# Optimization experiments

Hardware: AMD Instinct MI355X
Metric: run time of the kernel (lower is better)

Reference implementation:

```python
import jax, jax.numpy as jnp
import numpy as np

B = 65536        # batch
L = 1024         # input_size
K = 16           # filter_size
NUM_CLASSES = 4


def setup_inputs() -> dict:
    key = jax.random.key(0)
    k1, k2, k3, k4 = jax.random.split(key, 4)
    x = jax.random.normal(k1, (B, 1, L), dtype=jnp.float32)
    w = jax.random.normal(k2, (1, 1, K), dtype=jnp.float32) * 0.1
    b = jax.random.normal(k3, (1,), dtype=jnp.float32) * 0.1
    # per-class (lo, hi) intervals, lo <= hi, non-negative so sqrt fallback is real
    ranges = jnp.sort(jax.random.uniform(k4, (NUM_CLASSES, 2), dtype=jnp.float32) * 2.0, axis=1)
    return {"x": x, "w": w, "b": b, "ranges": ranges}


def reference(x, w, b, ranges):
    # Conv1d(1->1, K) + bias, ReLU, MaxPool1d over the full valid length -> [B,1,1]
    y = jax.lax.conv_general_dilated(
        x, w, window_strides=(1,), padding='VALID',
        dimension_numbers=('NCH', 'OIH', 'NCH'))
    y = jnp.maximum(y + b[None, :, None], 0.0)
    v = jnp.max(y, axis=-1, keepdims=True)            # [B,1,1]

    # vectorized replacement of Tensor.apply_(from_ranges_to_output)
    lo = ranges[:, 0]                                  # [4]
    hi = ranges[:, 1]                                  # [4]
    vv = v[..., None]                                  # [B,1,1,1]
    matches = (vv >= lo) & (vv <= hi)                  # [B,1,1,4]
    in_any = jnp.any(matches, axis=-1)                 # [B,1,1]
    first_match = jnp.argmax(matches, axis=-1)         # first i with v in [lo_i,hi_i]

    # fallback: distances (v^2 + bound)^0.5 over interleaved [lo0,hi0,lo1,hi1,...]
    flat_bounds = ranges.reshape(-1)                   # [8]
    dists = jnp.sqrt(vv * vv + flat_bounds)            # [B,1,1,8]
    fallback_label = jnp.argmin(dists, axis=-1) // 2   # [B,1,1]

    out = jnp.where(in_any, first_match, fallback_label).astype(jnp.uint8)
    return out
```

## Files before the change

### kernel.cpp

```cpp
#include <hip/hip_runtime.h>
#include <math.h>

#define BROWS 65536
#define LLEN  1024
#define KW    16
#define NPOS  (LLEN - KW + 1)
#define RPB   4
#define NBLOCKS 2048
#define ROWS_PER_WAVE (BROWS / (NBLOCKS * RPB))

typedef float f4 __attribute__((ext_vector_type(4)));

__device__ __forceinline__ void load_row(const float* __restrict__ xr,
                                         int fbase, float* __restrict__ buf) {
#pragma unroll
    for (int j = 0; j < 8; ++j) {
        int off = fbase + 4 * j;
        off = (off > LLEN - 4) ? (LLEN - 4) : off;
        *(f4*)(&buf[4 * j]) = *(const f4*)(xr + off);
    }
}

__device__ __forceinline__ float conv_max(const float* __restrict__ xv,
                                          const float* __restrict__ wv,
                                          int own) {
    float vmax = -INFINITY;
#pragma unroll
    for (int pp = 0; pp < KW; ++pp) {
        float acc = 0.0f;
#pragma unroll
        for (int k = 0; k < KW; ++k) acc = fmaf(xv[pp + k], wv[k], acc);
        if (own + pp < NPOS) vmax = fmaxf(vmax, acc);
    }
    return vmax;
}

__device__ __forceinline__ void finish_row(float vmax, int lane, float bv,
                                           const float* __restrict__ lo,
                                           const float* __restrict__ hi,
                                           int fb, int* __restrict__ out,
                                           int row) {
#pragma unroll
    for (int off = 32; off > 0; off >>= 1)
        vmax = fmaxf(vmax, __shfl_xor(vmax, off, 64));
    if (lane == 0) {
        const float v = fmaxf(vmax + bv, 0.0f);
        int label = fb;
#pragma unroll
        for (int j = 3; j >= 0; --j)
            label = (v >= lo[j] && v <= hi[j]) ? j : label;
        out[row] = label;
    }
}

__global__ __launch_bounds__(256) void conv_pool_classify(
    const float* __restrict__ x,
    const float* __restrict__ w,
    const float* __restrict__ bias,
    const float* __restrict__ ranges,
    int* __restrict__ out)
{
    const int lane  = threadIdx.x & 63;
    const int wid   = threadIdx.x >> 6;
    const int wave  = blockIdx.x * RPB + wid;
    const int row0  = wave * ROWS_PER_WAVE;
    const int fbase = 16 * lane;

    float wv[KW];
#pragma unroll
    for (int k = 0; k < KW; ++k) wv[k] = w[k];
    const float bv = bias[0];

    float rr[8];
#pragma unroll
    for (int j = 0; j < 8; ++j) rr[j] = ranges[j];
    int fb = 0; float bm = rr[0];
#pragma unroll
    for (int j = 1; j < 8; ++j) { if (rr[j] < bm) { bm = rr[j]; fb = j; } }
    fb >>= 1;
    const float lo[4] = {rr[0], rr[2], rr[4], rr[6]};
    const float hi[4] = {rr[1], rr[3], rr[5], rr[7]};

    float bufA[32], bufB[32];
    load_row(x + (size_t)row0 * LLEN, fbase, bufA);

#pragma unroll 1
    for (int it = 0; it < ROWS_PER_WAVE; it += 2) {
        load_row(x + (size_t)(row0 + it + 1) * LLEN, fbase, bufB);
        const float m0 = conv_max(bufA, wv, fbase);
        finish_row(m0, lane, bv, lo, hi, fb, out, row0 + it);

        if (it + 2 < ROWS_PER_WAVE)
            load_row(x + (size_t)(row0 + it + 2) * LLEN, fbase, bufA);
        const float m1 = conv_max(bufB, wv, fbase);
        finish_row(m1, lane, bv, lo, hi, fb, out, row0 + it + 1);
    }
}

extern "C" void kernel_launch(void* const* d_in, const int* in_sizes, int n_in,
                              void* d_out, int out_size, void* d_ws, size_t ws_size,
                              hipStream_t stream) {
    const float* x      = (const float*)d_in[0];
    const float* w      = (const float*)d_in[1];
    const float* bias   = (const float*)d_in[2];
    const float* ranges = (const float*)d_in[3];
    int* out = (int*)d_out;

    dim3 grid(NBLOCKS);
    dim3 block(256);
    conv_pool_classify<<<grid, block, 0, stream>>>(x, w, bias, ranges, out);
}
```

Measured before the change: 361.0 us.

## Stage rows through swizzled LDS with coalesced nontemporal loads and batched label stores

Each wave now loads a row with fully coalesced nontemporal float4 loads (64 lanes over contiguous 1 KB segments) instead of overlapping per-lane 128-byte windows. The data is written to a swizzled shared-memory tile, and each lane reads back its 32-float window for the 16-tap convolution. Labels are collected in one register per lane and written with a single store per wave. This is meant to cut redundant global traffic and improve coalescing, at the cost of LDS round trips and barrier-free reuse that relies on wave-local ordering.

```diff
diff --git a/kernel.cpp b/kernel.cpp
--- a/kernel.cpp
+++ b/kernel.cpp
@@ -9,49 +9,9 @@
 #define NBLOCKS 2048
 #define ROWS_PER_WAVE (BROWS / (NBLOCKS * RPB))
 
-typedef float f4 __attribute__((ext_vector_type(4)));
+typedef float nt_float4 __attribute__((ext_vector_type(4)));
 
-__device__ __forceinline__ void load_row(const float* __restrict__ xr,
-                                         int fbase, float* __restrict__ buf) {
-#pragma unroll
-    for (int j = 0; j < 8; ++j) {
-        int off = fbase + 4 * j;
-        off = (off > LLEN - 4) ? (LLEN - 4) : off;
-        *(f4*)(&buf[4 * j]) = *(const f4*)(xr + off);
-    }
-}
-
-__device__ __forceinline__ float conv_max(const float* __restrict__ xv,
-                                          const float* __restrict__ wv,
-                                          int own) {
-    float vmax = -INFINITY;
-#pragma unroll
-    for (int pp = 0; pp < KW; ++pp) {
-        float acc = 0.0f;
-#pragma unroll
-        for (int k = 0; k < KW; ++k) acc = fmaf(xv[pp + k], wv[k], acc);
-        if (own + pp < NPOS) vmax = fmaxf(vmax, acc);
-    }
-    return vmax;
-}
-
-__device__ __forceinline__ void finish_row(float vmax, int lane, float bv,
-                                           const float* __restrict__ lo,
-                                           const float* __restrict__ hi,
-                                           int fb, int* __restrict__ out,
-                                           int row) {
-#pragma unroll
-    for (int off = 32; off > 0; off >>= 1)
-        vmax = fmaxf(vmax, __shfl_xor(vmax, off, 64));
-    if (lane == 0) {
-        const float v = fmaxf(vmax + bv, 0.0f);
-        int label = fb;
-#pragma unroll
-        for (int j = 3; j >= 0; --j)
-            label = (v >= lo[j] && v <= hi[j]) ? j : label;
-        out[row] = label;
-    }
-}
+__device__ __forceinline__ int swz(int g) { return g ^ ((g >> 3) & 7); }
 
 __global__ __launch_bounds__(256) void conv_pool_classify(
     const float* __restrict__ x,
@@ -60,11 +20,12 @@
     const float* __restrict__ ranges,
     int* __restrict__ out)
 {
-    const int lane  = threadIdx.x & 63;
-    const int wid   = threadIdx.x >> 6;
-    const int wave  = blockIdx.x * RPB + wid;
-    const int row0  = wave * ROWS_PER_WAVE;
-    const int fbase = 16 * lane;
+    __shared__ nt_float4 lds[RPB][LLEN / 4];
+
+    const int lane = threadIdx.x & 63;
+    const int wid  = threadIdx.x >> 6;
+    const int wave = blockIdx.x * RPB + wid;
+    const int row0 = wave * ROWS_PER_WAVE;
 
     float wv[KW];
 #pragma unroll
@@ -81,20 +42,59 @@
     const float lo[4] = {rr[0], rr[2], rr[4], rr[6]};
     const float hi[4] = {rr[1], rr[3], rr[5], rr[7]};
 
-    float bufA[32], bufB[32];
-    load_row(x + (size_t)row0 * LLEN, fbase, bufA);
+    nt_float4 p[4];
+    {
+        const float* __restrict__ xr = x + (size_t)row0 * LLEN;
+#pragma unroll
+        for (int s = 0; s < 4; ++s)
+            p[s] = __builtin_nontemporal_load((const nt_float4*)(xr + 256 * s + 4 * lane));
+    }
 
-#pragma unroll 1
-    for (int it = 0; it < ROWS_PER_WAVE; it += 2) {
-        load_row(x + (size_t)(row0 + it + 1) * LLEN, fbase, bufB);
-        const float m0 = conv_max(bufA, wv, fbase);
-        finish_row(m0, lane, bv, lo, hi, fb, out, row0 + it);
+    int mylbl = 0;
 
-        if (it + 2 < ROWS_PER_WAVE)
-            load_row(x + (size_t)(row0 + it + 2) * LLEN, fbase, bufA);
-        const float m1 = conv_max(bufB, wv, fbase);
-        finish_row(m1, lane, bv, lo, hi, fb, out, row0 + it + 1);
+    for (int it = 0; it < ROWS_PER_WAVE; ++it) {
+#pragma unroll
+        for (int s = 0; s < 4; ++s)
+            lds[wid][swz(64 * s + lane)] = p[s];
+
+        if (it + 1 < ROWS_PER_WAVE) {
+            const float* __restrict__ xr = x + (size_t)(row0 + it + 1) * LLEN;
+#pragma unroll
+            for (int s = 0; s < 4; ++s)
+                p[s] = __builtin_nontemporal_load((const nt_float4*)(xr + 256 * s + 4 * lane));
+        }
+
+        float xv[32];
+#pragma unroll
+        for (int j = 0; j < 8; ++j) {
+            int g = 4 * lane + j;
+            if (g > 255) g = 255;
+            *(nt_float4*)(&xv[4 * j]) = lds[wid][swz(g)];
+        }
+
+        const int own = 16 * lane;
+        float vmax = -INFINITY;
+#pragma unroll
+        for (int pp = 0; pp < KW; ++pp) {
+            float acc = 0.0f;
+#pragma unroll
+            for (int k = 0; k < KW; ++k) acc = fmaf(xv[pp + k], wv[k], acc);
+            vmax = ((own + pp) < NPOS) ? fmaxf(vmax, acc) : vmax;
+        }
+
+#pragma unroll
+        for (int off = 32; off > 0; off >>= 1)
+            vmax = fmaxf(vmax, __shfl_xor(vmax, off, 64));
+
+        const float v = fmaxf(vmax + bv, 0.0f);
+        int label = fb;
+#pragma unroll
+        for (int j = 3; j >= 0; --j)
+            label = (v >= lo[j] && v <= hi[j]) ? j : label;
+        if (lane == it) mylbl = label;
     }
+
+    if (lane < ROWS_PER_WAVE) out[row0 + lane] = mylbl;
 }
 
 extern "C" void kernel_launch(void* const* d_in, const int* in_sizes, int n_in,
```

After: 337.8 us. -6.4%, faster.
